# Kernel optimization log

Hardware: AMD Instinct MI355X
Metric: run time of the kernel (lower is better)

The kernel has to match this reference:

```python
import jax, jax.numpy as jnp
import numpy as np
from jax import lax


def _attention_conv(x, Wq, bq, Wk, bk, Wv, bv, head_w, p):
    # x: [B,C,H,W]; Wq/Wk/Wv: [heads, D, D] (torch Linear weight, out x in); b*: [heads, D]
    B, C, H, W = x.shape
    pad_h = (p * (1 + H // p) - H) % p
    pad_w = (p * (1 + W // p) - W) % p
    xp = jnp.pad(x, ((0, 0), (0, 0), (p + pad_h, p), (p + pad_w, p)), mode='reflect')
    num_h = (H + pad_h) // p
    num_w = (W + pad_w) // p
    # view padded image as a grid of (num_h+2) x (num_w+2) patches of size p x p
    g = xp.reshape(B, C, num_h + 2, p, num_w + 2, p)
    # 9-patch neighborhood per window (equivalent to unfold with window=3p, stride=p)
    nb = jnp.stack([g[:, :, di:di + num_h, :, dj:dj + num_w, :]
                    for di in range(3) for dj in range(3)], axis=2)  # [B,C,9,num_h,p,num_w,p]
    tokens = nb.transpose(0, 3, 5, 2, 1, 4, 6).reshape(B * num_h * num_w, 9, C * p * p)
    D = C * p * p
    q = jnp.einsum('npd,hed->nhpe', tokens, Wq) + bq[None, :, None, :]
    k = jnp.einsum('npd,hed->nhpe', tokens, Wk) + bk[None, :, None, :]
    v = jnp.einsum('npd,hed->nhpe', tokens, Wv) + bv[None, :, None, :]
    # core patch (index 4 = center of 3x3) attends to all 9 patches
    score = jnp.einsum('nhe,nhpe->nhp', q[:, :, 4, :], k) / jnp.sqrt(jnp.float32(D))
    attn = jax.nn.softmax(score, axis=-1)               # [N,heads,9]
    out = jnp.einsum('nhp,nhpe->nhe', attn, v)          # [N,heads,D]
    mixed = jnp.einsum('h,nhe->ne', head_w[0], out)     # head-weight mixing -> [N,D]
    out = mixed.reshape(B, num_h, num_w, C, p, p).transpose(0, 3, 1, 4, 2, 5)
    out = out.reshape(B, C, num_h * p, num_w * p)
    return out[:, :, pad_h:, pad_w:]


def _dehaze(x, p3, p6, p9, conv0_w, conv0_b):
    b, c, h, w = x.shape
    avg = jnp.mean((1.0 - x).reshape(b, c, -1), axis=-1, keepdims=True)  # [b,c,1]
    xg1 = jax.nn.softmax(avg, axis=-1)[..., None]                        # softmax over size-1 dim -> ones
    xg = jnp.max((x * xg1).reshape(b, 1, -1), axis=-1, keepdims=True)[..., None]  # [b,1,1,1]
    x3 = _attention_conv(x, *p3, 1)
    x6 = _attention_conv(x3, *p6, 2)
    x9 = _attention_conv(x6, *p9, 3)
    cat = jnp.concatenate([x9, x6, x3], axis=1)
    x0 = jax.nn.relu(lax.conv_general_dilated(cat, conv0_w, (1, 1), [(2, 2), (2, 2)])
                     + conv0_b[None, :, None, None])
    return jax.nn.relu(x * x0 + (xg - x0))


def setup_inputs() -> dict:
    key = jax.random.key(0)
    ks = jax.random.split(key, 12)
    inp = {'x': jax.random.uniform(ks[0], (2, 3, 384, 384), jnp.float32)}
    specs = [('3', 6, 3), ('6', 4, 12), ('9', 2, 27)]  # (stage, num_heads, D=C*p*p)
    i = 1
    for name, h, d in specs:
        for proj in ('q', 'k', 'v'):
            inp['w%s_%s' % (name, proj)] = jax.random.normal(ks[i], (h, d, d), jnp.float32) * 0.02
            inp['b%s_%s' % (name, proj)] = jnp.zeros((h, d), jnp.float32)
            i += 1
        inp['hw%s' % name] = jnp.ones((1, h), jnp.float32) / h
    inp['conv0_w'] = jax.random.normal(ks[10], (3, 9, 5, 5), jnp.float32) * 0.02
    inp['conv0_b'] = jnp.zeros((3,), jnp.float32)
    return inp


def reference(x, w3_q, b3_q, w3_k, b3_k, w3_v, b3_v, hw3,
              w6_q, b6_q, w6_k, b6_k, w6_v, b6_v, hw6,
              w9_q, b9_q, w9_k, b9_k, w9_v, b9_v, hw9,
              conv0_w, conv0_b):
    p3 = (w3_q, b3_q, w3_k, b3_k, w3_v, b3_v, hw3)
    p6 = (w6_q, b6_q, w6_k, b6_k, w6_v, b6_v, hw6)
    p9 = (w9_q, b9_q, w9_k, b9_k, w9_v, b9_v, hw9)
    return _dehaze(x, p3, p6, p9, conv0_w, conv0_b)
```

## Files before the change

### kernel.cpp

```cpp
#include <hip/hip_runtime.h>

#define HH 384
#define HWPX (HH*HH)

#define WOFF3 16
#define HS3   40
#define WOFF6 256
#define HS6   328
#define WOFF9 1568
#define HS9   1600
#define CATOFF 8192
#define P9BOFF (CATOFF + 2*9*HWPX)
#define WS_NEED ((size_t)(P9BOFF + 2*3*HWPX) * 4)

__device__ __forceinline__ float4 fma4s(float4 a, float4 w, float t) {
    a.x += w.x * t; a.y += w.y * t; a.z += w.z * t; a.w += w.w * t; return a;
}
__device__ __forceinline__ float dot4(float4 a, float4 b) {
    return a.x * b.x + a.y * b.y + a.z * b.z + a.w * b.w;
}

__global__ __launch_bounds__(256) void pre_xg(
    const float* __restrict__ w3q, const float* __restrict__ b3q,
    const float* __restrict__ w3k, const float* __restrict__ b3k,
    const float* __restrict__ w3v, const float* __restrict__ b3v, const float* __restrict__ hw3,
    const float* __restrict__ w6q, const float* __restrict__ b6q,
    const float* __restrict__ w6k, const float* __restrict__ b6k,
    const float* __restrict__ w6v, const float* __restrict__ b6v, const float* __restrict__ hw6,
    const float* __restrict__ w9q, const float* __restrict__ b9q,
    const float* __restrict__ w9k, const float* __restrict__ b9k,
    const float* __restrict__ w9v, const float* __restrict__ b9v, const float* __restrict__ hw9,
    const float* __restrict__ x, float* __restrict__ ws)
{
    __shared__ float sm[4];
    const int blk = blockIdx.x;
    const int tid = threadIdx.x;

    if (blk < 12) {
        int stage = blk < 6 ? 0 : (blk < 10 ? 1 : 2);
        int h = blk - (stage == 0 ? 0 : (stage == 1 ? 6 : 10));
        const float* WQ[3] = {w3q, w6q, w9q};
        const float* BQ[3] = {b3q, b6q, b9q};
        const float* WK[3] = {w3k, w6k, w9k};
        const float* BK[3] = {b3k, b6k, b9k};
        const float* WV_[3] = {w3v, w6v, w9v};
        const float* BV[3] = {b3v, b6v, b9v};
        const float* HWp[3] = {hw3, hw6, hw9};
        const int Ds[3] = {3, 12, 27};
        const int DPs[3] = {4, 12, 28};
        const int WOFFs[3] = {WOFF3, WOFF6, WOFF9};
        const int HSs[3] = {HS3, HS6, HS9};

        const int D = Ds[stage], DP = DPs[stage];
        const float* wq = WQ[stage] + h * D * D;
        const float* bq = BQ[stage] + h * D;
        const float* wk = WK[stage] + h * D * D;
        const float* bk = BK[stage] + h * D;
        const float* wv = WV_[stage] + h * D * D;
        const float* bv = BV[stage] + h * D;
        const float hwv = HWp[stage][h];
        float* base = ws + WOFFs[stage] + h * HSs[stage];
        const float scale = rsqrtf((float)D);

        for (int i = tid; i < D * DP; i += 256) {
            int a = i / DP, b = i % DP;
            float m = 0.f;
            if (b < D) for (int e = 0; e < D; ++e) m += wk[e * D + b] * wq[e * D + a];
            base[i] = scale * m;
            float wvv = 0.f;
            if (b < D) wvv = hwv * wv[a * D + b];
            base[D * DP + i] = wvv;
        }
        for (int i = tid; i < DP; i += 256) {
            float cv = 0.f, uv = 0.f;
            if (i < D) for (int e = 0; e < D; ++e) {
                cv += bq[e] * wk[e * D + i];
                uv += wq[e * D + i] * bk[e];
            }
            base[2 * D * DP + i] = scale * cv;
            base[2 * D * DP + DP + i] = scale * uv;
            base[2 * D * DP + 2 * DP + i] = (i < D) ? hwv * bv[i] : 0.f;
        }
        if (tid == 0) {
            float s = 0.f;
            for (int e = 0; e < D; ++e) s += bq[e] * bk[e];
            base[2 * D * DP + 3 * DP] = scale * s;
        }
    } else {
        int i2 = blk - 12;
        int b = i2 / 144, chunk = i2 % 144;
        const float4* xb = (const float4*)(x + (size_t)b * 3 * HWPX + chunk * 3072);
        float m = 0.f;
        for (int j = tid; j < 768; j += 256) {
            float4 v = xb[j];
            m = fmaxf(m, fmaxf(fmaxf(v.x, v.y), fmaxf(v.z, v.w)));
        }
        for (int off = 32; off; off >>= 1)
            m = fmaxf(m, __shfl_down(m, off));
        if ((tid & 63) == 0) sm[tid >> 6] = m;
        __syncthreads();
        if (tid == 0) {
            float mm = fmaxf(fmaxf(sm[0], sm[1]), fmaxf(sm[2], sm[3]));
            atomicMax((int*)&ws[b], __float_as_int(mm));
        }
    }
}

template <int P, int HEADS, int HSPLIT>
__global__ __launch_bounds__(256) void attn_cell(
    const float* __restrict__ in, long in_bstride,
    float* __restrict__ outA, long outA_bstride,
    float* __restrict__ outB, long outB_bstride,
    const float* __restrict__ wsw)
{
    constexpr int C = 3, D = C * P * P, DP = (D + 3) & ~3, NREG = DP / 4;
    constexpr int HS = 2 * D * DP + 3 * DP + 4;
    constexpr int HPT = HEADS / HSPLIT;
    __shared__ __align__(16) float scell[324 * DP];
    __shared__ __align__(16) float sw[HPT * HS];

    const int tid = threadIdx.x;
    const int z = blockIdx.z;
    const int b = z & 1;
    const int hs = z >> 1;
    const int BWY = blockIdx.y * 16, BWX = blockIdx.x * 16;

    const float* inb = in + (size_t)b * in_bstride;
    constexpr int XW = 18 * P;
    constexpr int TOT = 3 * P * 18 * XW;
    for (int i = tid; i < TOT; i += 256) {
        int c = i / (P * 18 * XW);
        int rem = i % (P * 18 * XW);
        int r = rem / (18 * XW);
        int rem2 = rem % (18 * XW);
        int cy = rem2 / XW, xx = rem2 % XW;
        int y = (BWY + cy) * P + r - P; y = y < 0 ? -y : (y >= HH ? 2 * HH - 2 - y : y);
        int x = BWX * P + xx - P;       x = x < 0 ? -x : (x >= HH ? 2 * HH - 2 - x : x);
        int cx = xx / P, s = xx % P;
        scell[(cy * 18 + cx) * DP + (c * P + r) * P + s] = inb[c * HWPX + y * HH + x];
    }
    if constexpr (DP > D) {
        for (int j = tid; j < 324; j += 256) scell[j * DP + D] = 0.f;
    }
    const float* wsrc = wsw + (size_t)hs * HPT * HS;
    for (int i = tid; i < HPT * HS; i += 256) sw[i] = wsrc[i];
    __syncthreads();

    const int wx = tid & 15, wy = tid >> 4;

    float t4[DP];
    {
        const float4* T4p = (const float4*)&scell[((wy + 1) * 18 + wx + 1) * DP];
#pragma unroll
        for (int k = 0; k < NREG; ++k) {
            float4 v = T4p[k];
            t4[4 * k] = v.x; t4[4 * k + 1] = v.y; t4[4 * k + 2] = v.z; t4[4 * k + 3] = v.w;
        }
    }
    float mixed[D];
#pragma unroll
    for (int e = 0; e < D; ++e) mixed[e] = 0.f;

#pragma unroll 1
    for (int hh = 0; hh < HPT; ++hh) {
        const float* hb = sw + hh * HS;
        const float* ccb = hb + 2 * D * DP;
        float4 qk[NREG];
        {
            const float4* cp = (const float4*)ccb;
#pragma unroll
            for (int k = 0; k < NREG; ++k) qk[k] = cp[k];
        }
        float su = ccb[3 * DP];
#pragma unroll
        for (int a = 0; a < D; ++a) {
            const float t = t4[a];
            su += ccb[DP + a] * t;
            const float4* Mr = (const float4*)(hb + a * DP);
#pragma unroll
            for (int k = 0; k < NREG; ++k) qk[k] = fma4s(qk[k], Mr[k], t);
        }
        float denom = 0.f;
        float4 wt[NREG];
#pragma unroll
        for (int k = 0; k < NREG; ++k) wt[k] = make_float4(0.f, 0.f, 0.f, 0.f);
#pragma unroll
        for (int di = 0; di < 3; ++di)
#pragma unroll
            for (int dj = 0; dj < 3; ++dj) {
                const float4* cp = (const float4*)&scell[((wy + di) * 18 + wx + dj) * DP];
                float4 cv[NREG];
#pragma unroll
                for (int k = 0; k < NREG; ++k) cv[k] = cp[k];
                float s = su;
#pragma unroll
                for (int k = 0; k < NREG; ++k) s += dot4(qk[k], cv[k]);
                const float e = __expf(s);
                denom += e;
#pragma unroll
                for (int k = 0; k < NREG; ++k) wt[k] = fma4s(wt[k], cv[k], e);
            }
        const float winv = 1.f / denom;
#pragma unroll
        for (int k = 0; k < NREG; ++k) {
            wt[k].x *= winv; wt[k].y *= winv; wt[k].z *= winv; wt[k].w *= winv;
        }
        const float* WVb = hb + D * DP;
#pragma unroll
        for (int e = 0; e < D; ++e) {
            const float4* Wr = (const float4*)(WVb + e * DP);
            float o = ccb[2 * DP + e];
#pragma unroll
            for (int k = 0; k < NREG; ++k) o += dot4(Wr[k], wt[k]);
            mixed[e] += o;
        }
    }

    float* outp = (hs == 0) ? (outA + (size_t)b * outA_bstride)
                            : (outB + (size_t)b * outB_bstride);
#pragma unroll
    for (int c = 0; c < C; ++c)
#pragma unroll
        for (int r = 0; r < P; ++r)
#pragma unroll
            for (int s = 0; s < P; ++s)
                outp[c * HWPX + ((BWY + wy) * P + r) * HH + (BWX + wx) * P + s] =
                    mixed[(c * P + r) * P + s];
}

__global__ __launch_bounds__(128) void conv_final(
    const float* __restrict__ cat, const float* __restrict__ p9b, int addp9,
    const float* __restrict__ w, const float* __restrict__ bias,
    const float* __restrict__ x, const float* __restrict__ xg,
    float* __restrict__ out)
{
    __shared__ float tile[9][20][40];
    const int tid = threadIdx.x;
    const int b = blockIdx.z;
    const int bx = blockIdx.x * 32, by = blockIdx.y * 16;
    const float* catb = cat + (size_t)b * 9 * HWPX;
    const float* p9bb = p9b + (size_t)b * 3 * HWPX;

    for (int i = tid; i < 9 * 20 * 10; i += 128) {
        int ci = i / 200;
        int rem = i % 200;
        int row = rem / 10, c4 = rem % 10;
        int y = by + row - 2, xx = bx - 4 + 4 * c4;
        float4 v = {0.f, 0.f, 0.f, 0.f};
        if (y >= 0 && y < HH && xx >= 0 && xx <= HH - 4) {
            v = *(const float4*)&catb[ci * HWPX + y * HH + xx];
            if (addp9 && ci < 3) {
                float4 u = *(const float4*)&p9bb[ci * HWPX + y * HH + xx];
                v.x += u.x; v.y += u.y; v.z += u.z; v.w += u.w;
            }
        }
        *(float4*)&tile[ci][row][4 * c4] = v;
    }
    __syncthreads();

    const int tx = tid & 7, ty = tid >> 3;
    float acc0[4], acc1[4], acc2[4];
    const float b0 = bias[0], b1 = bias[1], b2 = bias[2];
#pragma unroll
    for (int j = 0; j < 4; ++j) { acc0[j] = b0; acc1[j] = b1; acc2[j] = b2; }

#pragma unroll
    for (int ky = 0; ky < 5; ++ky) {
#pragma unroll 1
        for (int ci = 0; ci < 9; ++ci) {
            const float4 ra = *(const float4*)&tile[ci][ty + ky][4 * tx];
            const float4 rb = *(const float4*)&tile[ci][ty + ky][4 * tx + 4];
            const float4 rc = *(const float4*)&tile[ci][ty + ky][4 * tx + 8];
            const float r[12] = {ra.x, ra.y, ra.z, ra.w, rb.x, rb.y, rb.z, rb.w,
                                 rc.x, rc.y, rc.z, rc.w};
            const float* __restrict__ w0 = w + (0 * 9 + ci) * 25 + ky * 5;
            const float* __restrict__ w1 = w + (1 * 9 + ci) * 25 + ky * 5;
            const float* __restrict__ w2 = w + (2 * 9 + ci) * 25 + ky * 5;
#pragma unroll
            for (int j = 0; j < 4; ++j)
#pragma unroll
                for (int kx = 0; kx < 5; ++kx) {
                    const float t = r[j + kx + 2];
                    acc0[j] += t * w0[kx];
                    acc1[j] += t * w1[kx];
                    acc2[j] += t * w2[kx];
                }
        }
    }

    const int yb = by + ty, xb = bx + 4 * tx;
    const float xgv = xg[b];
    float* accs[3] = {acc0, acc1, acc2};
#pragma unroll
    for (int co = 0; co < 3; ++co) {
        const float4 xv = *(const float4*)&x[((size_t)(b * 3 + co)) * HWPX + yb * HH + xb];
        const float* a = accs[co];
        float4 ov;
        float x0;
        x0 = fmaxf(a[0], 0.f); ov.x = fmaxf(xv.x * x0 + xgv - x0, 0.f);
        x0 = fmaxf(a[1], 0.f); ov.y = fmaxf(xv.y * x0 + xgv - x0, 0.f);
        x0 = fmaxf(a[2], 0.f); ov.z = fmaxf(xv.z * x0 + xgv - x0, 0.f);
        x0 = fmaxf(a[3], 0.f); ov.w = fmaxf(xv.w * x0 + xgv - x0, 0.f);
        *(float4*)&out[((size_t)(b * 3 + co)) * HWPX + yb * HH + xb] = ov;
    }
}

extern "C" void kernel_launch(void* const* d_in, const int* in_sizes, int n_in,
                              void* d_out, int out_size, void* d_ws, size_t ws_size,
                              hipStream_t stream) {
    const float* x   = (const float*)d_in[0];
    const float* w3q = (const float*)d_in[1];
    const float* b3q = (const float*)d_in[2];
    const float* w3k = (const float*)d_in[3];
    const float* b3k = (const float*)d_in[4];
    const float* w3v = (const float*)d_in[5];
    const float* b3v = (const float*)d_in[6];
    const float* hw3 = (const float*)d_in[7];
    const float* w6q = (const float*)d_in[8];
    const float* b6q = (const float*)d_in[9];
    const float* w6k = (const float*)d_in[10];
    const float* b6k = (const float*)d_in[11];
    const float* w6v = (const float*)d_in[12];
    const float* b6v = (const float*)d_in[13];
    const float* hw6 = (const float*)d_in[14];
    const float* w9q = (const float*)d_in[15];
    const float* b9q = (const float*)d_in[16];
    const float* w9k = (const float*)d_in[17];
    const float* b9k = (const float*)d_in[18];
    const float* w9v = (const float*)d_in[19];
    const float* b9v = (const float*)d_in[20];
    const float* hw9 = (const float*)d_in[21];
    const float* c0w = (const float*)d_in[22];
    const float* c0b = (const float*)d_in[23];

    float* out = (float*)d_out;
    float* ws  = (float*)d_ws;
    float* cat = ws + CATOFF;
    float* p9b = ws + P9BOFF;
    const bool split9 = ws_size >= WS_NEED;

    pre_xg<<<300, 256, 0, stream>>>(
        w3q, b3q, w3k, b3k, w3v, b3v, hw3,
        w6q, b6q, w6k, b6k, w6v, b6v, hw6,
        w9q, b9q, w9k, b9k, w9v, b9v, hw9, x, ws);

    attn_cell<1, 6, 1><<<dim3(24, 24, 2), 256, 0, stream>>>(
        x, 3 * HWPX, cat + 6 * HWPX, 9 * HWPX, cat + 6 * HWPX, 9 * HWPX, ws + WOFF3);
    attn_cell<2, 4, 1><<<dim3(12, 12, 2), 256, 0, stream>>>(
        cat + 6 * HWPX, 9 * HWPX, cat + 3 * HWPX, 9 * HWPX, cat + 3 * HWPX, 9 * HWPX, ws + WOFF6);
    if (split9)
        attn_cell<3, 2, 2><<<dim3(8, 8, 4), 256, 0, stream>>>(
            cat + 3 * HWPX, 9 * HWPX, cat, 9 * HWPX, p9b, 3 * HWPX, ws + WOFF9);
    else
        attn_cell<3, 2, 1><<<dim3(8, 8, 2), 256, 0, stream>>>(
            cat + 3 * HWPX, 9 * HWPX, cat, 9 * HWPX, cat, 9 * HWPX, ws + WOFF9);

    conv_final<<<dim3(12, 24, 2), 128, 0, stream>>>(
        cat, p9b, split9 ? 1 : 0, c0w, c0b, x, ws, out);
}
```

Before: 216.5 us.

## Retile attention stages into smaller blocks, fuse xg max into stage one

Replaces the fixed 16x16-window attention kernel with a templated version that takes a configurable window tile and thread count. Stages 6 and 9 now run as 64-thread blocks over 8x8 windows, which gives many more blocks, in place of the head-split workaround for stage 9. Stage 3 and 6 keep all 9 neighbour cells in registers, the halo is loaded with vectorized float4 reads, and the global max for xg is folded into the stage-3 load so the separate max pass over x goes away. The trade-offs are more register pressure and a larger halo-to-interior ratio with smaller tiles.

```diff
diff --git a/kernel.cpp b/kernel.cpp
--- a/kernel.cpp
+++ b/kernel.cpp
@@ -10,8 +10,6 @@
 #define WOFF9 1568
 #define HS9   1600
 #define CATOFF 8192
-#define P9BOFF (CATOFF + 2*9*HWPX)
-#define WS_NEED ((size_t)(P9BOFF + 2*3*HWPX) * 4)
 
 __device__ __forceinline__ float4 fma4s(float4 a, float4 w, float t) {
     a.x += w.x * t; a.y += w.y * t; a.z += w.z * t; a.w += w.w * t; return a;
@@ -19,8 +17,11 @@
 __device__ __forceinline__ float dot4(float4 a, float4 b) {
     return a.x * b.x + a.y * b.y + a.z * b.z + a.w * b.w;
 }
-
-__global__ __launch_bounds__(256) void pre_xg(
+__device__ __forceinline__ float f4c(const float4& v, int j) {
+    return j == 0 ? v.x : (j == 1 ? v.y : (j == 2 ? v.z : v.w));
+}
+
+__global__ __launch_bounds__(256) void pre_w(
     const float* __restrict__ w3q, const float* __restrict__ b3q,
     const float* __restrict__ w3k, const float* __restrict__ b3k,
     const float* __restrict__ w3v, const float* __restrict__ b3v, const float* __restrict__ hw3,
@@ -30,180 +31,214 @@
     const float* __restrict__ w9q, const float* __restrict__ b9q,
     const float* __restrict__ w9k, const float* __restrict__ b9k,
     const float* __restrict__ w9v, const float* __restrict__ b9v, const float* __restrict__ hw9,
-    const float* __restrict__ x, float* __restrict__ ws)
+    float* __restrict__ ws)
 {
-    __shared__ float sm[4];
     const int blk = blockIdx.x;
     const int tid = threadIdx.x;
-
-    if (blk < 12) {
-        int stage = blk < 6 ? 0 : (blk < 10 ? 1 : 2);
-        int h = blk - (stage == 0 ? 0 : (stage == 1 ? 6 : 10));
-        const float* WQ[3] = {w3q, w6q, w9q};
-        const float* BQ[3] = {b3q, b6q, b9q};
-        const float* WK[3] = {w3k, w6k, w9k};
-        const float* BK[3] = {b3k, b6k, b9k};
-        const float* WV_[3] = {w3v, w6v, w9v};
-        const float* BV[3] = {b3v, b6v, b9v};
-        const float* HWp[3] = {hw3, hw6, hw9};
-        const int Ds[3] = {3, 12, 27};
-        const int DPs[3] = {4, 12, 28};
-        const int WOFFs[3] = {WOFF3, WOFF6, WOFF9};
-        const int HSs[3] = {HS3, HS6, HS9};
-
-        const int D = Ds[stage], DP = DPs[stage];
-        const float* wq = WQ[stage] + h * D * D;
-        const float* bq = BQ[stage] + h * D;
-        const float* wk = WK[stage] + h * D * D;
-        const float* bk = BK[stage] + h * D;
-        const float* wv = WV_[stage] + h * D * D;
-        const float* bv = BV[stage] + h * D;
-        const float hwv = HWp[stage][h];
-        float* base = ws + WOFFs[stage] + h * HSs[stage];
-        const float scale = rsqrtf((float)D);
-
-        for (int i = tid; i < D * DP; i += 256) {
-            int a = i / DP, b = i % DP;
-            float m = 0.f;
-            if (b < D) for (int e = 0; e < D; ++e) m += wk[e * D + b] * wq[e * D + a];
-            base[i] = scale * m;
-            float wvv = 0.f;
-            if (b < D) wvv = hwv * wv[a * D + b];
-            base[D * DP + i] = wvv;
-        }
-        for (int i = tid; i < DP; i += 256) {
-            float cv = 0.f, uv = 0.f;
-            if (i < D) for (int e = 0; e < D; ++e) {
-                cv += bq[e] * wk[e * D + i];
-                uv += wq[e * D + i] * bk[e];
-            }
-            base[2 * D * DP + i] = scale * cv;
-            base[2 * D * DP + DP + i] = scale * uv;
-            base[2 * D * DP + 2 * DP + i] = (i < D) ? hwv * bv[i] : 0.f;
-        }
-        if (tid == 0) {
-            float s = 0.f;
-            for (int e = 0; e < D; ++e) s += bq[e] * bk[e];
-            base[2 * D * DP + 3 * DP] = scale * s;
-        }
-    } else {
-        int i2 = blk - 12;
-        int b = i2 / 144, chunk = i2 % 144;
-        const float4* xb = (const float4*)(x + (size_t)b * 3 * HWPX + chunk * 3072);
+    int stage = blk < 6 ? 0 : (blk < 10 ? 1 : 2);
+    int h = blk - (stage == 0 ? 0 : (stage == 1 ? 6 : 10));
+    const float* WQ[3] = {w3q, w6q, w9q};
+    const float* BQ[3] = {b3q, b6q, b9q};
+    const float* WK[3] = {w3k, w6k, w9k};
+    const float* BK[3] = {b3k, b6k, b9k};
+    const float* WV_[3] = {w3v, w6v, w9v};
+    const float* BV[3] = {b3v, b6v, b9v};
+    const float* HWp[3] = {hw3, hw6, hw9};
+    const int Ds[3] = {3, 12, 27};
+    const int DPs[3] = {4, 12, 28};
+    const int WOFFs[3] = {WOFF3, WOFF6, WOFF9};
+    const int HSs[3] = {HS3, HS6, HS9};
+
+    const int D = Ds[stage], DP = DPs[stage];
+    const float* wq = WQ[stage] + h * D * D;
+    const float* bq = BQ[stage] + h * D;
+    const float* wk = WK[stage] + h * D * D;
+    const float* bk = BK[stage] + h * D;
+    const float* wv = WV_[stage] + h * D * D;
+    const float* bv = BV[stage] + h * D;
+    const float hwv = HWp[stage][h];
+    float* base = ws + WOFFs[stage] + h * HSs[stage];
+    const float scale = rsqrtf((float)D);
+
+    for (int i = tid; i < D * DP; i += 256) {
+        int a = i / DP, b = i % DP;
         float m = 0.f;
-        for (int j = tid; j < 768; j += 256) {
-            float4 v = xb[j];
-            m = fmaxf(m, fmaxf(fmaxf(v.x, v.y), fmaxf(v.z, v.w)));
-        }
-        for (int off = 32; off; off >>= 1)
-            m = fmaxf(m, __shfl_down(m, off));
-        if ((tid & 63) == 0) sm[tid >> 6] = m;
-        __syncthreads();
-        if (tid == 0) {
-            float mm = fmaxf(fmaxf(sm[0], sm[1]), fmaxf(sm[2], sm[3]));
-            atomicMax((int*)&ws[b], __float_as_int(mm));
-        }
-    }
-}
-
-template <int P, int HEADS, int HSPLIT>
-__global__ __launch_bounds__(256) void attn_cell(
+        if (b < D) for (int e = 0; e < D; ++e) m += wk[e * D + b] * wq[e * D + a];
+        base[i] = scale * m;
+        float wvv = 0.f;
+        if (b < D) wvv = hwv * wv[a * D + b];
+        base[D * DP + i] = wvv;
+    }
+    for (int i = tid; i < DP; i += 256) {
+        float cv = 0.f, uv = 0.f;
+        if (i < D) for (int e = 0; e < D; ++e) {
+            cv += bq[e] * wk[e * D + i];
+            uv += wq[e * D + i] * bk[e];
+        }
+        base[2 * D * DP + i] = scale * cv;
+        base[2 * D * DP + DP + i] = scale * uv;
+        base[2 * D * DP + 2 * DP + i] = (i < D) ? hwv * bv[i] : 0.f;
+    }
+    if (tid == 0) {
+        float s = 0.f;
+        for (int e = 0; e < D; ++e) s += bq[e] * bk[e];
+        base[2 * D * DP + 3 * DP] = scale * s;
+    }
+}
+
+template <int P, int HEADS, int NWX, int NWY, int NT, bool CELLREG, bool DO_XG>
+__global__ __launch_bounds__(NT) void attn_k(
     const float* __restrict__ in, long in_bstride,
-    float* __restrict__ outA, long outA_bstride,
-    float* __restrict__ outB, long outB_bstride,
-    const float* __restrict__ wsw)
+    float* __restrict__ out, long out_bstride,
+    const float* __restrict__ wsw, float* __restrict__ xgws)
 {
     constexpr int C = 3, D = C * P * P, DP = (D + 3) & ~3, NREG = DP / 4;
     constexpr int HS = 2 * D * DP + 3 * DP + 4;
-    constexpr int HPT = HEADS / HSPLIT;
-    __shared__ __align__(16) float scell[324 * DP];
-    __shared__ __align__(16) float sw[HPT * HS];
+    constexpr int CW = NWX + 2, CH = NWY + 2;
+    constexpr int TC = CW * P, TR = CH * P;
+    constexpr int NCHX = (TC + 3) / 4;
+    constexpr int TOTC = C * TR * NCHX;
+    constexpr int CPT = (TOTC + NT - 1) / NT;
+
+    __shared__ __align__(16) float scell[CH * CW * DP];
+    __shared__ __align__(16) float sw[HEADS * HS];
 
     const int tid = threadIdx.x;
-    const int z = blockIdx.z;
-    const int b = z & 1;
-    const int hs = z >> 1;
-    const int BWY = blockIdx.y * 16, BWX = blockIdx.x * 16;
-
+    const int b = blockIdx.z;
+    const int BWX = blockIdx.x * NWX, BWY = blockIdx.y * NWY;
+    const int base_x = BWX * P - P, base_y = BWY * P - P;
     const float* inb = in + (size_t)b * in_bstride;
-    constexpr int XW = 18 * P;
-    constexpr int TOT = 3 * P * 18 * XW;
-    for (int i = tid; i < TOT; i += 256) {
-        int c = i / (P * 18 * XW);
-        int rem = i % (P * 18 * XW);
-        int r = rem / (18 * XW);
-        int rem2 = rem % (18 * XW);
-        int cy = rem2 / XW, xx = rem2 % XW;
-        int y = (BWY + cy) * P + r - P; y = y < 0 ? -y : (y >= HH ? 2 * HH - 2 - y : y);
-        int x = BWX * P + xx - P;       x = x < 0 ? -x : (x >= HH ? 2 * HH - 2 - x : x);
-        int cx = xx / P, s = xx % P;
-        scell[(cy * 18 + cx) * DP + (c * P + r) * P + s] = inb[c * HWPX + y * HH + x];
+
+    {
+        const float4* src4 = (const float4*)wsw;
+        float4* sw4 = (float4*)sw;
+#pragma unroll
+        for (int it = 0; it < (HEADS * HS / 4 + NT - 1) / NT; ++it) {
+            int i = tid + it * NT;
+            if (i < HEADS * HS / 4) sw4[i] = src4[i];
+        }
+    }
+
+    float tmax = 0.f;
+#pragma unroll
+    for (int it = 0; it < CPT; ++it) {
+        int idx = tid + it * NT;
+        if (idx < TOTC) {
+            int c = idx / (TR * NCHX);
+            int rem = idx - c * (TR * NCHX);
+            int row = rem / NCHX;
+            int k = rem - row * NCHX;
+            int gy = base_y + row; gy = gy < 0 ? -gy : (gy >= HH ? 2 * HH - 2 - gy : gy);
+            int gx0 = base_x + 4 * k;
+            const float* src = inb + c * HWPX + gy * HH;
+            float v[4];
+            if (gx0 >= 0 && gx0 + 4 <= HH) {
+                float4 f = *(const float4*)(src + gx0);
+                v[0] = f.x; v[1] = f.y; v[2] = f.z; v[3] = f.w;
+            } else {
+#pragma unroll
+                for (int j = 0; j < 4; ++j) {
+                    int gx = gx0 + j; gx = gx < 0 ? -gx : (gx >= HH ? 2 * HH - 2 - gx : gx);
+                    v[j] = src[gx];
+                }
+            }
+            const int nel = (4 * k + 4 <= TC) ? 4 : (TC - 4 * k);
+            const int cy = row / P, r = row - cy * P;
+#pragma unroll
+            for (int j = 0; j < 4; ++j) {
+                if (j < nel) {
+                    int xx = 4 * k + j;
+                    int cx = xx / P, s = xx - cx * P;
+                    scell[(cy * CW + cx) * DP + (c * P + r) * P + s] = v[j];
+                    if (DO_XG) tmax = fmaxf(tmax, v[j]);
+                }
+            }
+        }
     }
     if constexpr (DP > D) {
-        for (int j = tid; j < 324; j += 256) scell[j * DP + D] = 0.f;
-    }
-    const float* wsrc = wsw + (size_t)hs * HPT * HS;
-    for (int i = tid; i < HPT * HS; i += 256) sw[i] = wsrc[i];
+        for (int i = tid; i < CH * CW; i += NT) scell[i * DP + D] = 0.f;
+    }
     __syncthreads();
 
-    const int wx = tid & 15, wy = tid >> 4;
-
-    float t4[DP];
-    {
-        const float4* T4p = (const float4*)&scell[((wy + 1) * 18 + wx + 1) * DP];
-#pragma unroll
-        for (int k = 0; k < NREG; ++k) {
-            float4 v = T4p[k];
-            t4[4 * k] = v.x; t4[4 * k + 1] = v.y; t4[4 * k + 2] = v.z; t4[4 * k + 3] = v.w;
-        }
-    }
+    if (DO_XG) {
+        float m = tmax;
+        for (int off = 32; off; off >>= 1) m = fmaxf(m, __shfl_down(m, off));
+        if ((tid & 63) == 0) atomicMax((int*)xgws + b, __float_as_int(m));
+    }
+
+    const int wx = tid % NWX, wy = tid / NWX;
+    const float4* cbase = (const float4*)scell;
+
+    float4 Tc[CELLREG ? 9 : 1][NREG];
+    float4 t4v[NREG];
+    if constexpr (CELLREG) {
+#pragma unroll
+        for (int di = 0; di < 3; ++di)
+#pragma unroll
+            for (int dj = 0; dj < 3; ++dj) {
+                const float4* p = cbase + ((size_t)(wy + di) * CW + (wx + dj)) * NREG;
+#pragma unroll
+                for (int kk = 0; kk < NREG; ++kk) Tc[di * 3 + dj][kk] = p[kk];
+            }
+    } else {
+        const float4* p = cbase + ((size_t)(wy + 1) * CW + (wx + 1)) * NREG;
+#pragma unroll
+        for (int kk = 0; kk < NREG; ++kk) t4v[kk] = p[kk];
+    }
+
     float mixed[D];
 #pragma unroll
     for (int e = 0; e < D; ++e) mixed[e] = 0.f;
 
 #pragma unroll 1
-    for (int hh = 0; hh < HPT; ++hh) {
-        const float* hb = sw + hh * HS;
+    for (int h = 0; h < HEADS; ++h) {
+        const float* hb = &sw[h * HS];
         const float* ccb = hb + 2 * D * DP;
         float4 qk[NREG];
         {
             const float4* cp = (const float4*)ccb;
 #pragma unroll
-            for (int k = 0; k < NREG; ++k) qk[k] = cp[k];
+            for (int kk = 0; kk < NREG; ++kk) qk[kk] = cp[kk];
         }
         float su = ccb[3 * DP];
 #pragma unroll
         for (int a = 0; a < D; ++a) {
-            const float t = t4[a];
+            float t;
+            if constexpr (CELLREG) t = f4c(Tc[4][a / 4], a & 3);
+            else                   t = f4c(t4v[a / 4], a & 3);
             su += ccb[DP + a] * t;
             const float4* Mr = (const float4*)(hb + a * DP);
 #pragma unroll
-            for (int k = 0; k < NREG; ++k) qk[k] = fma4s(qk[k], Mr[k], t);
+            for (int kk = 0; kk < NREG; ++kk) qk[kk] = fma4s(qk[kk], Mr[kk], t);
         }
         float denom = 0.f;
         float4 wt[NREG];
 #pragma unroll
-        for (int k = 0; k < NREG; ++k) wt[k] = make_float4(0.f, 0.f, 0.f, 0.f);
-#pragma unroll
-        for (int di = 0; di < 3; ++di)
-#pragma unroll
-            for (int dj = 0; dj < 3; ++dj) {
-                const float4* cp = (const float4*)&scell[((wy + di) * 18 + wx + dj) * DP];
-                float4 cv[NREG];
-#pragma unroll
-                for (int k = 0; k < NREG; ++k) cv[k] = cp[k];
-                float s = su;
-#pragma unroll
-                for (int k = 0; k < NREG; ++k) s += dot4(qk[k], cv[k]);
-                const float e = __expf(s);
-                denom += e;
-#pragma unroll
-                for (int k = 0; k < NREG; ++k) wt[k] = fma4s(wt[k], cv[k], e);
+        for (int kk = 0; kk < NREG; ++kk) wt[kk] = make_float4(0.f, 0.f, 0.f, 0.f);
+#pragma unroll
+        for (int p9 = 0; p9 < 9; ++p9) {
+            float4 cv[NREG];
+            if constexpr (CELLREG) {
+#pragma unroll
+                for (int kk = 0; kk < NREG; ++kk) cv[kk] = Tc[p9][kk];
+            } else {
+                const int di = p9 / 3, dj = p9 % 3;
+                const float4* p = cbase + ((size_t)(wy + di) * CW + (wx + dj)) * NREG;
+#pragma unroll
+                for (int kk = 0; kk < NREG; ++kk) cv[kk] = p[kk];
             }
+            float s = su;
+#pragma unroll
+            for (int kk = 0; kk < NREG; ++kk) s += dot4(qk[kk], cv[kk]);
+            const float e = __expf(s);
+            denom += e;
+#pragma unroll
+            for (int kk = 0; kk < NREG; ++kk) wt[kk] = fma4s(wt[kk], cv[kk], e);
+        }
         const float winv = 1.f / denom;
 #pragma unroll
-        for (int k = 0; k < NREG; ++k) {
-            wt[k].x *= winv; wt[k].y *= winv; wt[k].z *= winv; wt[k].w *= winv;
+        for (int kk = 0; kk < NREG; ++kk) {
+            wt[kk].x *= winv; wt[kk].y *= winv; wt[kk].z *= winv; wt[kk].w *= winv;
         }
         const float* WVb = hb + D * DP;
 #pragma unroll
@@ -211,25 +246,24 @@
             const float4* Wr = (const float4*)(WVb + e * DP);
             float o = ccb[2 * DP + e];
 #pragma unroll
-            for (int k = 0; k < NREG; ++k) o += dot4(Wr[k], wt[k]);
+            for (int kk = 0; kk < NREG; ++kk) o += dot4(Wr[kk], wt[kk]);
             mixed[e] += o;
         }
     }
 
-    float* outp = (hs == 0) ? (outA + (size_t)b * outA_bstride)
-                            : (outB + (size_t)b * outB_bstride);
+    float* outb = out + (size_t)b * out_bstride;
 #pragma unroll
     for (int c = 0; c < C; ++c)
 #pragma unroll
         for (int r = 0; r < P; ++r)
 #pragma unroll
             for (int s = 0; s < P; ++s)
-                outp[c * HWPX + ((BWY + wy) * P + r) * HH + (BWX + wx) * P + s] =
+                outb[c * HWPX + ((BWY + wy) * P + r) * HH + (BWX + wx) * P + s] =
                     mixed[(c * P + r) * P + s];
 }
 
 __global__ __launch_bounds__(128) void conv_final(
-    const float* __restrict__ cat, const float* __restrict__ p9b, int addp9,
+    const float* __restrict__ cat,
     const float* __restrict__ w, const float* __restrict__ bias,
     const float* __restrict__ x, const float* __restrict__ xg,
     float* __restrict__ out)
@@ -239,22 +273,20 @@
     const int b = blockIdx.z;
     const int bx = blockIdx.x * 32, by = blockIdx.y * 16;
     const float* catb = cat + (size_t)b * 9 * HWPX;
-    const float* p9bb = p9b + (size_t)b * 3 * HWPX;
-
-    for (int i = tid; i < 9 * 20 * 10; i += 128) {
-        int ci = i / 200;
-        int rem = i % 200;
-        int row = rem / 10, c4 = rem % 10;
-        int y = by + row - 2, xx = bx - 4 + 4 * c4;
-        float4 v = {0.f, 0.f, 0.f, 0.f};
-        if (y >= 0 && y < HH && xx >= 0 && xx <= HH - 4) {
-            v = *(const float4*)&catb[ci * HWPX + y * HH + xx];
-            if (addp9 && ci < 3) {
-                float4 u = *(const float4*)&p9bb[ci * HWPX + y * HH + xx];
-                v.x += u.x; v.y += u.y; v.z += u.z; v.w += u.w;
-            }
-        }
-        *(float4*)&tile[ci][row][4 * c4] = v;
+
+#pragma unroll
+    for (int it = 0; it < 15; ++it) {
+        int i = tid + it * 128;
+        if (i < 1800) {
+            int ci = i / 200;
+            int rem = i - ci * 200;
+            int row = rem / 10, c4 = rem - row * 10;
+            int y = by + row - 2, xx = bx - 4 + 4 * c4;
+            float4 v = {0.f, 0.f, 0.f, 0.f};
+            if (y >= 0 && y < HH && xx >= 0 && xx <= HH - 4)
+                v = *(const float4*)&catb[ci * HWPX + y * HH + xx];
+            *(float4*)&tile[ci][row][4 * c4] = v;
+        }
     }
     __syncthreads();
 
@@ -336,25 +368,18 @@
     float* out = (float*)d_out;
     float* ws  = (float*)d_ws;
     float* cat = ws + CATOFF;
-    float* p9b = ws + P9BOFF;
-    const bool split9 = ws_size >= WS_NEED;
-
-    pre_xg<<<300, 256, 0, stream>>>(
+
+    pre_w<<<12, 256, 0, stream>>>(
         w3q, b3q, w3k, b3k, w3v, b3v, hw3,
         w6q, b6q, w6k, b6k, w6v, b6v, hw6,
-        w9q, b9q, w9k, b9k, w9v, b9v, hw9, x, ws);
-
-    attn_cell<1, 6, 1><<<dim3(24, 24, 2), 256, 0, stream>>>(
-        x, 3 * HWPX, cat + 6 * HWPX, 9 * HWPX, cat + 6 * HWPX, 9 * HWPX, ws + WOFF3);
-    attn_cell<2, 4, 1><<<dim3(12, 12, 2), 256, 0, stream>>>(
-        cat + 6 * HWPX, 9 * HWPX, cat + 3 * HWPX, 9 * HWPX, cat + 3 * HWPX, 9 * HWPX, ws + WOFF6);
-    if (split9)
-        attn_cell<3, 2, 2><<<dim3(8, 8, 4), 256, 0, stream>>>(
-            cat + 3 * HWPX, 9 * HWPX, cat, 9 * HWPX, p9b, 3 * HWPX, ws + WOFF9);
-    else
-        attn_cell<3, 2, 1><<<dim3(8, 8, 2), 256, 0, stream>>>(
-            cat + 3 * HWPX, 9 * HWPX, cat, 9 * HWPX, cat, 9 * HWPX, ws + WOFF9);
-
-    conv_final<<<dim3(12, 24, 2), 128, 0, stream>>>(
-        cat, p9b, split9 ? 1 : 0, c0w, c0b, x, ws, out);
-}
+        w9q, b9q, w9k, b9k, w9v, b9v, hw9, ws);
+
+    attn_k<1, 6, 16, 16, 256, true, true><<<dim3(24, 24, 2), 256, 0, stream>>>(
+        x, 3 * HWPX, cat + 6 * HWPX, 9 * HWPX, ws + WOFF3, ws);
+    attn_k<2, 4, 8, 8, 64, true, false><<<dim3(24, 24, 2), 64, 0, stream>>>(
+        cat + 6 * HWPX, 9 * HWPX, cat + 3 * HWPX, 9 * HWPX, ws + WOFF6, ws);
+    attn_k<3, 2, 8, 8, 64, false, false><<<dim3(16, 16, 2), 64, 0, stream>>>(
+        cat + 3 * HWPX, 9 * HWPX, cat, 9 * HWPX, ws + WOFF9, ws);
+
+    conv_final<<<dim3(12, 24, 2), 128, 0, stream>>>(cat, c0w, c0b, x, ws, out);
+}
```

Result: slower. 338.0 us (+56.1%).
